# Kernel tuning notes

Hardware: AMD Instinct MI355X
Metric: run time of the kernel (lower is better)

The kernel has to match this reference:

```python
import jax, jax.numpy as jnp
import numpy as np

N = 50000

def gcn_conv(x, src, dst, W, b, num_nodes):
    # x: [N, Fin], src/dst: [E'] (self-loops already included)
    h = x @ W  # [N, Fout]
    ones = jnp.ones(src.shape[0], dtype=h.dtype)
    deg = jax.ops.segment_sum(ones, dst, num_segments=num_nodes)  # in-degree incl. self-loop
    dinv = jnp.where(deg > 0, jax.lax.rsqrt(deg), 0.0)
    norm = dinv[src] * dinv[dst]  # [E']
    msg = h[src] * norm[:, None]  # gather + scale
    out = jax.ops.segment_sum(msg, dst, num_segments=num_nodes)  # scatter-add
    return out + b

def setup_inputs() -> dict:
    key = jax.random.key(0)
    k1, k2, k3, k4, k5, k6 = jax.random.split(key, 6)
    E = 800000
    Fin, H, Fout = 128, 64, 32
    x = jax.random.normal(k1, (N, Fin), dtype=jnp.float32)
    edge_index = jax.random.randint(k2, (2, E), 0, N, dtype=jnp.int32)
    edge_attr = jax.random.normal(k3, (E, 8), dtype=jnp.float32)
    s1 = 1.0 / np.sqrt(Fin)
    s2 = 1.0 / np.sqrt(H)
    W1 = jax.random.uniform(k4, (Fin, H), dtype=jnp.float32, minval=-s1, maxval=s1)
    b1 = jnp.zeros((H,), dtype=jnp.float32)
    W2 = jax.random.uniform(k5, (H, Fout), dtype=jnp.float32, minval=-s2, maxval=s2)
    b2 = jnp.zeros((Fout,), dtype=jnp.float32)
    return {"x": x, "edge_index": edge_index, "edge_attr": edge_attr,
            "W1": W1, "b1": b1, "W2": W2, "b2": b2}

def reference(x, edge_index, edge_attr, W1, b1, W2, b2):
    num_nodes = x.shape[0]
    loop = jnp.arange(num_nodes, dtype=edge_index.dtype)
    src = jnp.concatenate([edge_index[0], loop])
    dst = jnp.concatenate([edge_index[1], loop])
    h = gcn_conv(x, src, dst, W1, b1, num_nodes)
    h = jax.nn.relu(h)
    # dropout is identity in eval mode
    out = gcn_conv(h, src, dst, W2, b2, num_nodes)
    return out
```

## Files before the change

### kernel.cpp

```cpp
#include <hip/hip_runtime.h>
#include <hip/hip_fp16.h>
#include <cstdint>
#include <cstddef>


#define SHIFT 8
#define NPB 256
#define CHUNK 8192
#define IMG_CAP 6144

__global__ __launch_bounds__(256) void hist_kernel(const int* __restrict__ dst, int E, int nWG,
                                                   int B, int* __restrict__ hist) {
  __shared__ int h[256];
  int t = threadIdx.x, w = blockIdx.x;
  for (int i = t; i < B; i += 256) h[i] = 0;
  __syncthreads();
  int beg = w * CHUNK, end = min(beg + CHUNK, E);
  for (int i = beg + t; i < end; i += 256) atomicAdd(&h[dst[i] >> SHIFT], 1);
  __syncthreads();
  for (int i = t; i < B; i += 256) hist[i * nWG + w] = h[i];
}

__global__ __launch_bounds__(256) void rowscan_kernel(const int* __restrict__ hist, int nWG,
                                                      int* __restrict__ rowscan, int* __restrict__ total) {
  int b = blockIdx.x, t = threadIdx.x;
  int v = (t < nWG) ? hist[b * nWG + t] : 0;
  int lane = t & 63, wid = t >> 6;
  int x = v;
#pragma unroll
  for (int o = 1; o < 64; o <<= 1) { int y = __shfl_up(x, o, 64); if (lane >= o) x += y; }
  __shared__ int wsum[4];
  if (lane == 63) wsum[wid] = x;
  __syncthreads();
  int bw = 0;
  for (int i = 0; i < wid; ++i) bw += wsum[i];
  int incl = bw + x;
  if (t < nWG) rowscan[b * nWG + t] = incl - v;
  if (t == nWG - 1) total[b] = incl;
}

__global__ __launch_bounds__(256) void scatterkeys_kernel(const int* __restrict__ src,
                                                          const int* __restrict__ dst, int E, int nWG,
                                                          int B, const int* __restrict__ hist,
                                                          const int* __restrict__ rowscan,
                                                          const int* __restrict__ total,
                                                          unsigned* __restrict__ keys) {
  __shared__ int loffs[256], cur[256], gb[256];
  __shared__ int wsum[4];
  __shared__ unsigned image[CHUNK];
  __shared__ int gdst[CHUNK];
  int t = threadIdx.x, w = blockIdx.x;
  int lane = t & 63, wid = t >> 6;
  {
    int v = (t < B) ? total[t] : 0;
    int x = v;
#pragma unroll
    for (int o = 1; o < 64; o <<= 1) { int y = __shfl_up(x, o, 64); if (lane >= o) x += y; }
    if (lane == 63) wsum[wid] = x;
    __syncthreads();
    int bw = 0;
    for (int i = 0; i < wid; ++i) bw += wsum[i];
    int excl = bw + x - v;
    if (t < B) gb[t] = excl + rowscan[t * nWG + w];
  }
  __syncthreads();
  {
    int v = (t < B) ? hist[t * nWG + w] : 0;
    int x = v;
#pragma unroll
    for (int o = 1; o < 64; o <<= 1) { int y = __shfl_up(x, o, 64); if (lane >= o) x += y; }
    if (lane == 63) wsum[wid] = x;
    __syncthreads();
    int bw = 0;
    for (int i = 0; i < wid; ++i) bw += wsum[i];
    int excl = bw + x - v;
    if (t < B) { loffs[t] = excl; cur[t] = excl; }
  }
  __syncthreads();
  int beg = w * CHUNK, end = min(beg + CHUNK, E);
  for (int i = beg + t; i < end; i += 256) {
    int d = dst[i], s = src[i];
    int b = d >> SHIFT;
    int p = atomicAdd(&cur[b], 1);
    image[p] = ((unsigned)(d & (NPB - 1)) << 16) | (unsigned)s;
    gdst[p] = gb[b] + (p - loffs[b]);
  }
  __syncthreads();
  int n = end - beg;
  for (int i = t; i < n; i += 256) keys[gdst[i]] = image[i];
}

__global__ __launch_bounds__(256) void bucket_build_kernel(const unsigned* __restrict__ keys,
                                                           const int* __restrict__ total, int B, int N,
                                                           int* __restrict__ csr, int* __restrict__ eoff,
                                                           int* __restrict__ ecnt, float* __restrict__ dinv) {
  __shared__ int cnt[NPB], loffs[NPB], cur[NPB];
  __shared__ int red[4];
  __shared__ int image[IMG_CAP];
  int b = blockIdx.x, t = threadIdx.x;
  int lane = t & 63, wid = t >> 6;
  int part = 0;
  for (int i = t; i < b; i += 256) part += total[i];
#pragma unroll
  for (int o = 32; o > 0; o >>= 1) part += __shfl_down(part, o, 64);
  if (lane == 0) red[wid] = part;
  __syncthreads();
  int gbeg = red[0] + red[1] + red[2] + red[3];
  int m = total[b];
  int gend = gbeg + m;
  int nb = b << SHIFT;
  int nn = min(NPB, N - nb);
  cnt[t] = 0;
  __syncthreads();
  for (int i = gbeg + t; i < gend; i += 256) atomicAdd(&cnt[keys[i] >> 16], 1);
  __syncthreads();
  if (t < 64) {
    int v0 = cnt[4 * t], v1 = cnt[4 * t + 1], v2 = cnt[4 * t + 2], v3 = cnt[4 * t + 3];
    int s = v0 + v1 + v2 + v3, x = s;
#pragma unroll
    for (int o = 1; o < 64; o <<= 1) { int y = __shfl_up(x, o, 64); if (t >= o) x += y; }
    int e = x - s;
    loffs[4 * t] = e;                 cur[4 * t] = e;
    loffs[4 * t + 1] = e + v0;        cur[4 * t + 1] = e + v0;
    loffs[4 * t + 2] = e + v0 + v1;   cur[4 * t + 2] = e + v0 + v1;
    loffs[4 * t + 3] = e + v0 + v1 + v2; cur[4 * t + 3] = e + v0 + v1 + v2;
  }
  __syncthreads();
  for (int n2 = t; n2 < nn; n2 += 256) {
    eoff[nb + n2] = gbeg + loffs[n2];
    ecnt[nb + n2] = cnt[n2];
    dinv[nb + n2] = 1.0f / sqrtf((float)(cnt[n2] + 1));
  }
  if (m <= IMG_CAP) {
    for (int i = gbeg + t; i < gend; i += 256) {
      unsigned k = keys[i];
      int p = atomicAdd(&cur[k >> 16], 1);
      image[p] = (int)(k & 0xFFFFu);
    }
    __syncthreads();
    for (int i = t; i < m; i += 256) csr[gbeg + i] = image[i];
  } else {
    for (int i = gbeg + t; i < gend; i += 256) {
      unsigned k = keys[i];
      int p = atomicAdd(&cur[k >> 16], 1);
      csr[gbeg + p] = (int)(k & 0xFFFFu);
    }
  }
}

__global__ __launch_bounds__(256) void gemm1_kernel(
    const float* __restrict__ x, const float* __restrict__ W1,
    const float* __restrict__ dinv, __half* __restrict__ h1s, int N) {
  __shared__ float ws[128 * 64];
  __shared__ float xs[64 * 128];
  const int t = threadIdx.x;
  const int rowBase = blockIdx.x * 64;
  float4* ws4 = (float4*)ws;
  float4* xs4 = (float4*)xs;
  for (int i = t; i < 128 * 16; i += 256) ws4[i] = ((const float4*)W1)[i];
  for (int i = t; i < 64 * 32; i += 256) {
    int r = i >> 5, kq = i & 31;
    int row = rowBase + r;
    float4 v = make_float4(0.f, 0.f, 0.f, 0.f);
    if (row < N) v = ((const float4*)x)[(size_t)row * 32 + kq];
    xs4[r * 32 + (kq ^ ((r >> 2) & 7))] = v;
  }
  __syncthreads();
  const int g = t & 15;
  const int rg = t >> 4;
  const int swz = rg & 7;
  float acc[4][4] = {};
  for (int kq = 0; kq < 32; ++kq) {
    float4 a[4];
#pragma unroll
    for (int j = 0; j < 4; ++j) a[j] = xs4[(4 * rg + j) * 32 + (kq ^ swz)];
    float4 w[4];
#pragma unroll
    for (int kk = 0; kk < 4; ++kk) w[kk] = ws4[(4 * kq + kk) * 16 + g];
#pragma unroll
    for (int j = 0; j < 4; ++j) {
      acc[j][0] += a[j].x * w[0].x + a[j].y * w[1].x + a[j].z * w[2].x + a[j].w * w[3].x;
      acc[j][1] += a[j].x * w[0].y + a[j].y * w[1].y + a[j].z * w[2].y + a[j].w * w[3].y;
      acc[j][2] += a[j].x * w[0].z + a[j].y * w[1].z + a[j].z * w[2].z + a[j].w * w[3].z;
      acc[j][3] += a[j].x * w[0].w + a[j].y * w[1].w + a[j].z * w[2].w + a[j].w * w[3].w;
    }
  }
#pragma unroll
  for (int j = 0; j < 4; ++j) {
    int row = rowBase + 4 * rg + j;
    if (row < N) {
      float dv = dinv[row];
      union { __half2 h2[2]; float2 f2v; } u;
      u.h2[0] = __floats2half2_rn(acc[j][0] * dv, acc[j][1] * dv);
      u.h2[1] = __floats2half2_rn(acc[j][2] * dv, acc[j][3] * dv);
      ((float2*)h1s)[(size_t)row * 16 + g] = u.f2v;
    }
  }
}

__global__ __launch_bounds__(256) void gather64_gemm2_kernel(
    const __half* __restrict__ h1s, const int* __restrict__ csr, const int* __restrict__ eoff,
    const int* __restrict__ ecnt, const float* __restrict__ dinv, const float* __restrict__ b1,
    const float* __restrict__ W2, __half* __restrict__ h2s, int N) {
  __shared__ float w2s[64 * 32];
  __shared__ float arow[8 * 64];
  int t = threadIdx.x;
  float4* w2s4 = (float4*)w2s;
  for (int i = t; i < 512; i += 256) w2s4[i] = ((const float4*)W2)[i];
  __syncthreads();
  int slot = t >> 5;
  int d = blockIdx.x * 8 + slot;
  if (d >= N) return;
  int f2 = t & 31;
  const __half2* h1p = (const __half2*)h1s;
  int beg = eoff[d], m = ecnt[d];
  float2 a0 = __half22float2(h1p[(size_t)d * 32 + f2]);
  float2 aA = make_float2(0.f, 0.f), aB = make_float2(0.f, 0.f), aC = make_float2(0.f, 0.f);
  int j = 0;
  for (; j + 16 <= m; j += 16) {
    int s[16];
#pragma unroll
    for (int i = 0; i < 16; ++i) s[i] = csr[beg + j + i];
    __half2 v[16];
#pragma unroll
    for (int i = 0; i < 16; ++i) v[i] = h1p[(size_t)s[i] * 32 + f2];
#pragma unroll
    for (int i = 0; i < 16; ++i) {
      float2 f = __half22float2(v[i]);
      float2* ac = (i & 3) == 0 ? &a0 : (i & 3) == 1 ? &aA : (i & 3) == 2 ? &aB : &aC;
      ac->x += f.x; ac->y += f.y;
    }
  }
  for (; j + 4 <= m; j += 4) {
    int s0 = csr[beg + j], s1 = csr[beg + j + 1], s2 = csr[beg + j + 2], s3 = csr[beg + j + 3];
    __half2 v0 = h1p[(size_t)s0 * 32 + f2], v1 = h1p[(size_t)s1 * 32 + f2];
    __half2 v2 = h1p[(size_t)s2 * 32 + f2], v3 = h1p[(size_t)s3 * 32 + f2];
    float2 f0 = __half22float2(v0), f1 = __half22float2(v1);
    float2 f2v = __half22float2(v2), f3 = __half22float2(v3);
    a0.x += f0.x; a0.y += f0.y; aA.x += f1.x; aA.y += f1.y;
    aB.x += f2v.x; aB.y += f2v.y; aC.x += f3.x; aC.y += f3.y;
  }
  for (; j < m; ++j) {
    float2 f = __half22float2(h1p[(size_t)csr[beg + j] * 32 + f2]);
    a0.x += f.x; a0.y += f.y;
  }
  float sx = (a0.x + aA.x) + (aB.x + aC.x);
  float sy = (a0.y + aA.y) + (aB.y + aC.y);
  float dv = dinv[d];
  float2 bb = ((const float2*)b1)[f2];
  float ax = fmaxf(sx * dv + bb.x, 0.f);
  float ay = fmaxf(sy * dv + bb.y, 0.f);
  ((float2*)arow)[slot * 32 + f2] = make_float2(ax, ay);
  const float* ar = &arow[slot * 64];
  float s = 0.f;
#pragma unroll
  for (int kk = 0; kk < 64; ++kk) s += ar[kk] * w2s[kk * 32 + f2];
  h2s[(size_t)d * 32 + f2] = __float2half_rn(s * dv);
}

__global__ __launch_bounds__(256) void gather32_kernel(
    const __half* __restrict__ h2s, const int* __restrict__ csr, const int* __restrict__ eoff,
    const int* __restrict__ ecnt, const float* __restrict__ dinv, const float* __restrict__ b2,
    float* __restrict__ out, int N) {
  int t = threadIdx.x;
  int d = blockIdx.x * 16 + (t >> 4);
  if (d >= N) return;
  int f2 = t & 15;
  const __half2* h2p = (const __half2*)h2s;
  int beg = eoff[d], m = ecnt[d];
  float2 a0 = __half22float2(h2p[(size_t)d * 16 + f2]);
  float2 aA = make_float2(0.f, 0.f), aB = make_float2(0.f, 0.f), aC = make_float2(0.f, 0.f);
  int j = 0;
  for (; j + 16 <= m; j += 16) {
    int s[16];
#pragma unroll
    for (int i = 0; i < 16; ++i) s[i] = csr[beg + j + i];
    __half2 v[16];
#pragma unroll
    for (int i = 0; i < 16; ++i) v[i] = h2p[(size_t)s[i] * 16 + f2];
#pragma unroll
    for (int i = 0; i < 16; ++i) {
      float2 f = __half22float2(v[i]);
      float2* ac = (i & 3) == 0 ? &a0 : (i & 3) == 1 ? &aA : (i & 3) == 2 ? &aB : &aC;
      ac->x += f.x; ac->y += f.y;
    }
  }
  for (; j + 4 <= m; j += 4) {
    int s0 = csr[beg + j], s1 = csr[beg + j + 1], s2 = csr[beg + j + 2], s3 = csr[beg + j + 3];
    __half2 v0 = h2p[(size_t)s0 * 16 + f2], v1 = h2p[(size_t)s1 * 16 + f2];
    __half2 v2 = h2p[(size_t)s2 * 16 + f2], v3 = h2p[(size_t)s3 * 16 + f2];
    float2 f0 = __half22float2(v0), f1 = __half22float2(v1);
    float2 f2v = __half22float2(v2), f3 = __half22float2(v3);
    a0.x += f0.x; a0.y += f0.y; aA.x += f1.x; aA.y += f1.y;
    aB.x += f2v.x; aB.y += f2v.y; aC.x += f3.x; aC.y += f3.y;
  }
  for (; j < m; ++j) {
    float2 f = __half22float2(h2p[(size_t)csr[beg + j] * 16 + f2]);
    a0.x += f.x; a0.y += f.y;
  }
  float sx = (a0.x + aA.x) + (aB.x + aC.x);
  float sy = (a0.y + aA.y) + (aB.y + aC.y);
  float dv = dinv[d];
  float2 bb = ((const float2*)b2)[f2];
  ((float2*)out)[(size_t)d * 16 + f2] = make_float2(sx * dv + bb.x, sy * dv + bb.y);
}

extern "C" void kernel_launch(void* const* d_in, const int* in_sizes, int n_in,
                              void* d_out, int out_size, void* d_ws, size_t ws_size,
                              hipStream_t stream) {
  const float* x = (const float*)d_in[0];
  const int* edge_index = (const int*)d_in[1];
  const float* W1 = (const float*)d_in[3];
  const float* b1 = (const float*)d_in[4];
  const float* W2 = (const float*)d_in[5];
  const float* b2 = (const float*)d_in[6];
  float* out = (float*)d_out;

  const int N = in_sizes[0] / 128;
  const int E = in_sizes[1] / 2;
  const int* src = edge_index;
  const int* dst = edge_index + E;

  const int B = (N + NPB - 1) >> SHIFT;
  const int nWG = (E + CHUNK - 1) / CHUNK;

  char* ws = (char*)d_ws;
  size_t off = 0;
  auto alloc = [&](size_t bytes) -> void* {
    void* p = ws + off;
    off += (bytes + 255) & ~(size_t)255;
    return p;
  };
  unsigned* keys = (unsigned*)alloc((size_t)E * 4);
  int* csr = (int*)alloc((size_t)E * 4);
  int* hist = (int*)alloc((size_t)B * nWG * 4);
  int* rowscan = (int*)alloc((size_t)B * nWG * 4);
  int* total = (int*)alloc((size_t)B * 4);
  int* eoff = (int*)alloc((size_t)N * 4);
  int* ecnt = (int*)alloc((size_t)N * 4);
  float* dinv = (float*)alloc((size_t)N * 4);
  __half* h1s = (__half*)alloc((size_t)N * 64 * 2);
  __half* h2s = (__half*)alloc((size_t)N * 32 * 2);

  hist_kernel<<<nWG, 256, 0, stream>>>(dst, E, nWG, B, hist);
  rowscan_kernel<<<B, 256, 0, stream>>>(hist, nWG, rowscan, total);
  scatterkeys_kernel<<<nWG, 256, 0, stream>>>(src, dst, E, nWG, B, hist, rowscan, total, keys);
  bucket_build_kernel<<<B, 256, 0, stream>>>(keys, total, B, N, csr, eoff, ecnt, dinv);
  gemm1_kernel<<<(N + 63) / 64, 256, 0, stream>>>(x, W1, dinv, h1s, N);
  gather64_gemm2_kernel<<<(N + 7) / 8, 256, 0, stream>>>(h1s, csr, eoff, ecnt, dinv, b1, W2, h2s, N);
  gather32_kernel<<<(N + 15) / 16, 256, 0, stream>>>(h2s, csr, eoff, ecnt, dinv, b2, out, N);
}
```

Before: 107.2 us.

## Drop rowscan kernel, use 16-bit CSR indices, widen gather64 loads

Removes the separate rowscan kernel: scatterkeys and bucket_build now recompute bucket totals and prefix offsets by scanning each histogram row themselves. The bucket id is packed into the upper bits of each key, so the gdst shared array is no longer needed, and CHUNK is halved. CSR source indices are stored as 16-bit values, which halves index traffic in both gathers but caps node ids at 65535. gather64 now gives each thread 4 halves per load with 16 threads per node. The cost is redundant serial scans of the histogram row per thread.

```diff
diff --git a/kernel.cpp b/kernel.cpp
--- a/kernel.cpp
+++ b/kernel.cpp
@@ -6,7 +6,7 @@
 
 #define SHIFT 8
 #define NPB 256
-#define CHUNK 8192
+#define CHUNK 4096
 #define IMG_CAP 6144
 
 __global__ __launch_bounds__(256) void hist_kernel(const int* __restrict__ dst, int E, int nWG,
@@ -21,60 +21,45 @@
   for (int i = t; i < B; i += 256) hist[i * nWG + w] = h[i];
 }
 
-__global__ __launch_bounds__(256) void rowscan_kernel(const int* __restrict__ hist, int nWG,
-                                                      int* __restrict__ rowscan, int* __restrict__ total) {
-  int b = blockIdx.x, t = threadIdx.x;
-  int v = (t < nWG) ? hist[b * nWG + t] : 0;
-  int lane = t & 63, wid = t >> 6;
-  int x = v;
-#pragma unroll
-  for (int o = 1; o < 64; o <<= 1) { int y = __shfl_up(x, o, 64); if (lane >= o) x += y; }
-  __shared__ int wsum[4];
-  if (lane == 63) wsum[wid] = x;
-  __syncthreads();
-  int bw = 0;
-  for (int i = 0; i < wid; ++i) bw += wsum[i];
-  int incl = bw + x;
-  if (t < nWG) rowscan[b * nWG + t] = incl - v;
-  if (t == nWG - 1) total[b] = incl;
-}
-
 __global__ __launch_bounds__(256) void scatterkeys_kernel(const int* __restrict__ src,
                                                           const int* __restrict__ dst, int E, int nWG,
                                                           int B, const int* __restrict__ hist,
-                                                          const int* __restrict__ rowscan,
-                                                          const int* __restrict__ total,
                                                           unsigned* __restrict__ keys) {
   __shared__ int loffs[256], cur[256], gb[256];
   __shared__ int wsum[4];
   __shared__ unsigned image[CHUNK];
-  __shared__ int gdst[CHUNK];
   int t = threadIdx.x, w = blockIdx.x;
   int lane = t & 63, wid = t >> 6;
+  int tot = 0, rp = 0, myc = 0;
+  if (t < B) {
+    const int* row = hist + (size_t)t * nWG;
+    for (int w2 = 0; w2 < nWG; ++w2) {
+      int v = row[w2];
+      tot += v;
+      if (w2 < w) rp += v;
+      if (w2 == w) myc = v;
+    }
+  }
   {
-    int v = (t < B) ? total[t] : 0;
-    int x = v;
+    int x = tot;
 #pragma unroll
     for (int o = 1; o < 64; o <<= 1) { int y = __shfl_up(x, o, 64); if (lane >= o) x += y; }
     if (lane == 63) wsum[wid] = x;
     __syncthreads();
     int bw = 0;
     for (int i = 0; i < wid; ++i) bw += wsum[i];
-    int excl = bw + x - v;
-    if (t < B) gb[t] = excl + rowscan[t * nWG + w];
+    if (t < B) gb[t] = bw + x - tot + rp;
   }
   __syncthreads();
   {
-    int v = (t < B) ? hist[t * nWG + w] : 0;
-    int x = v;
+    int x = myc;
 #pragma unroll
     for (int o = 1; o < 64; o <<= 1) { int y = __shfl_up(x, o, 64); if (lane >= o) x += y; }
     if (lane == 63) wsum[wid] = x;
     __syncthreads();
     int bw = 0;
     for (int i = 0; i < wid; ++i) bw += wsum[i];
-    int excl = bw + x - v;
-    if (t < B) { loffs[t] = excl; cur[t] = excl; }
+    if (t < B) { loffs[t] = bw + x - myc; cur[t] = bw + x - myc; }
   }
   __syncthreads();
   int beg = w * CHUNK, end = min(beg + CHUNK, E);
@@ -82,37 +67,51 @@
     int d = dst[i], s = src[i];
     int b = d >> SHIFT;
     int p = atomicAdd(&cur[b], 1);
-    image[p] = ((unsigned)(d & (NPB - 1)) << 16) | (unsigned)s;
-    gdst[p] = gb[b] + (p - loffs[b]);
+    image[p] = ((unsigned)b << 24) | ((unsigned)(d & (NPB - 1)) << 16) | (unsigned)s;
   }
   __syncthreads();
   int n = end - beg;
-  for (int i = t; i < n; i += 256) keys[gdst[i]] = image[i];
+  for (int i = t; i < n; i += 256) {
+    unsigned k = image[i];
+    int b = (int)(k >> 24);
+    keys[gb[b] + (i - loffs[b])] = k;
+  }
 }
 
 __global__ __launch_bounds__(256) void bucket_build_kernel(const unsigned* __restrict__ keys,
-                                                           const int* __restrict__ total, int B, int N,
-                                                           int* __restrict__ csr, int* __restrict__ eoff,
-                                                           int* __restrict__ ecnt, float* __restrict__ dinv) {
+                                                           const int* __restrict__ hist, int nWG,
+                                                           int B, int N,
+                                                           unsigned short* __restrict__ csr,
+                                                           int* __restrict__ eoff,
+                                                           int* __restrict__ ecnt,
+                                                           float* __restrict__ dinv) {
   __shared__ int cnt[NPB], loffs[NPB], cur[NPB];
+  __shared__ int tsum[256];
   __shared__ int red[4];
   __shared__ int image[IMG_CAP];
   int b = blockIdx.x, t = threadIdx.x;
   int lane = t & 63, wid = t >> 6;
+  int tot = 0;
+  if (t < B) {
+    const int* row = hist + (size_t)t * nWG;
+    for (int w2 = 0; w2 < nWG; ++w2) tot += row[w2];
+  }
+  tsum[t] = tot;
+  __syncthreads();
   int part = 0;
-  for (int i = t; i < b; i += 256) part += total[i];
+  for (int i = t; i < b; i += 256) part += tsum[i];
 #pragma unroll
   for (int o = 32; o > 0; o >>= 1) part += __shfl_down(part, o, 64);
   if (lane == 0) red[wid] = part;
   __syncthreads();
   int gbeg = red[0] + red[1] + red[2] + red[3];
-  int m = total[b];
+  int m = tsum[b];
   int gend = gbeg + m;
   int nb = b << SHIFT;
   int nn = min(NPB, N - nb);
   cnt[t] = 0;
   __syncthreads();
-  for (int i = gbeg + t; i < gend; i += 256) atomicAdd(&cnt[keys[i] >> 16], 1);
+  for (int i = gbeg + t; i < gend; i += 256) atomicAdd(&cnt[(keys[i] >> 16) & 0xFF], 1);
   __syncthreads();
   if (t < 64) {
     int v0 = cnt[4 * t], v1 = cnt[4 * t + 1], v2 = cnt[4 * t + 2], v3 = cnt[4 * t + 3];
@@ -134,16 +133,16 @@
   if (m <= IMG_CAP) {
     for (int i = gbeg + t; i < gend; i += 256) {
       unsigned k = keys[i];
-      int p = atomicAdd(&cur[k >> 16], 1);
+      int p = atomicAdd(&cur[(k >> 16) & 0xFF], 1);
       image[p] = (int)(k & 0xFFFFu);
     }
     __syncthreads();
-    for (int i = t; i < m; i += 256) csr[gbeg + i] = image[i];
+    for (int i = t; i < m; i += 256) csr[gbeg + i] = (unsigned short)image[i];
   } else {
     for (int i = gbeg + t; i < gend; i += 256) {
       unsigned k = keys[i];
-      int p = atomicAdd(&cur[k >> 16], 1);
-      csr[gbeg + p] = (int)(k & 0xFFFFu);
+      int p = atomicAdd(&cur[(k >> 16) & 0xFF], 1);
+      csr[gbeg + p] = (unsigned short)(k & 0xFFFFu);
     }
   }
 }
@@ -199,68 +198,91 @@
 }
 
 __global__ __launch_bounds__(256) void gather64_gemm2_kernel(
-    const __half* __restrict__ h1s, const int* __restrict__ csr, const int* __restrict__ eoff,
-    const int* __restrict__ ecnt, const float* __restrict__ dinv, const float* __restrict__ b1,
+    const __half* __restrict__ h1s, const unsigned short* __restrict__ csr,
+    const int* __restrict__ eoff, const int* __restrict__ ecnt,
+    const float* __restrict__ dinv, const float* __restrict__ b1,
     const float* __restrict__ W2, __half* __restrict__ h2s, int N) {
   __shared__ float w2s[64 * 32];
-  __shared__ float arow[8 * 64];
+  __shared__ float arow[16 * 64];
   int t = threadIdx.x;
   float4* w2s4 = (float4*)w2s;
   for (int i = t; i < 512; i += 256) w2s4[i] = ((const float4*)W2)[i];
   __syncthreads();
-  int slot = t >> 5;
-  int d = blockIdx.x * 8 + slot;
+  int slot = t >> 4;
+  int d = blockIdx.x * 16 + slot;
   if (d >= N) return;
-  int f2 = t & 31;
-  const __half2* h1p = (const __half2*)h1s;
+  int f = t & 15;
+  const float2* h1p = (const float2*)h1s;
   int beg = eoff[d], m = ecnt[d];
-  float2 a0 = __half22float2(h1p[(size_t)d * 32 + f2]);
-  float2 aA = make_float2(0.f, 0.f), aB = make_float2(0.f, 0.f), aC = make_float2(0.f, 0.f);
+  float acc[4][4] = {};
+  {
+    union { float2 f2v; __half2 h2[2]; } u;
+    u.f2v = h1p[(size_t)d * 16 + f];
+    float2 lo = __half22float2(u.h2[0]), hi = __half22float2(u.h2[1]);
+    acc[0][0] = lo.x; acc[0][1] = lo.y; acc[0][2] = hi.x; acc[0][3] = hi.y;
+  }
   int j = 0;
   for (; j + 16 <= m; j += 16) {
-    int s[16];
-#pragma unroll
-    for (int i = 0; i < 16; ++i) s[i] = csr[beg + j + i];
-    __half2 v[16];
-#pragma unroll
-    for (int i = 0; i < 16; ++i) v[i] = h1p[(size_t)s[i] * 32 + f2];
+    int s_[16];
+#pragma unroll
+    for (int i = 0; i < 16; ++i) s_[i] = csr[beg + j + i];
+    float2 v_[16];
+#pragma unroll
+    for (int i = 0; i < 16; ++i) v_[i] = h1p[(size_t)s_[i] * 16 + f];
 #pragma unroll
     for (int i = 0; i < 16; ++i) {
-      float2 f = __half22float2(v[i]);
-      float2* ac = (i & 3) == 0 ? &a0 : (i & 3) == 1 ? &aA : (i & 3) == 2 ? &aB : &aC;
-      ac->x += f.x; ac->y += f.y;
+      union { float2 f2v; __half2 h2[2]; } u; u.f2v = v_[i];
+      float2 lo = __half22float2(u.h2[0]), hi = __half22float2(u.h2[1]);
+      acc[i & 3][0] += lo.x; acc[i & 3][1] += lo.y; acc[i & 3][2] += hi.x; acc[i & 3][3] += hi.y;
     }
   }
   for (; j + 4 <= m; j += 4) {
-    int s0 = csr[beg + j], s1 = csr[beg + j + 1], s2 = csr[beg + j + 2], s3 = csr[beg + j + 3];
-    __half2 v0 = h1p[(size_t)s0 * 32 + f2], v1 = h1p[(size_t)s1 * 32 + f2];
-    __half2 v2 = h1p[(size_t)s2 * 32 + f2], v3 = h1p[(size_t)s3 * 32 + f2];
-    float2 f0 = __half22float2(v0), f1 = __half22float2(v1);
-    float2 f2v = __half22float2(v2), f3 = __half22float2(v3);
-    a0.x += f0.x; a0.y += f0.y; aA.x += f1.x; aA.y += f1.y;
-    aB.x += f2v.x; aB.y += f2v.y; aC.x += f3.x; aC.y += f3.y;
+    int s_[4];
+#pragma unroll
+    for (int i = 0; i < 4; ++i) s_[i] = csr[beg + j + i];
+    float2 v_[4];
+#pragma unroll
+    for (int i = 0; i < 4; ++i) v_[i] = h1p[(size_t)s_[i] * 16 + f];
+#pragma unroll
+    for (int i = 0; i < 4; ++i) {
+      union { float2 f2v; __half2 h2[2]; } u; u.f2v = v_[i];
+      float2 lo = __half22float2(u.h2[0]), hi = __half22float2(u.h2[1]);
+      acc[i][0] += lo.x; acc[i][1] += lo.y; acc[i][2] += hi.x; acc[i][3] += hi.y;
+    }
   }
   for (; j < m; ++j) {
-    float2 f = __half22float2(h1p[(size_t)csr[beg + j] * 32 + f2]);
-    a0.x += f.x; a0.y += f.y;
-  }
-  float sx = (a0.x + aA.x) + (aB.x + aC.x);
-  float sy = (a0.y + aA.y) + (aB.y + aC.y);
+    union { float2 f2v; __half2 h2[2]; } u;
+    u.f2v = h1p[(size_t)csr[beg + j] * 16 + f];
+    float2 lo = __half22float2(u.h2[0]), hi = __half22float2(u.h2[1]);
+    acc[0][0] += lo.x; acc[0][1] += lo.y; acc[0][2] += hi.x; acc[0][3] += hi.y;
+  }
+  float g0 = (acc[0][0] + acc[1][0]) + (acc[2][0] + acc[3][0]);
+  float g1 = (acc[0][1] + acc[1][1]) + (acc[2][1] + acc[3][1]);
+  float g2 = (acc[0][2] + acc[1][2]) + (acc[2][2] + acc[3][2]);
+  float g3 = (acc[0][3] + acc[1][3]) + (acc[2][3] + acc[3][3]);
   float dv = dinv[d];
-  float2 bb = ((const float2*)b1)[f2];
-  float ax = fmaxf(sx * dv + bb.x, 0.f);
-  float ay = fmaxf(sy * dv + bb.y, 0.f);
-  ((float2*)arow)[slot * 32 + f2] = make_float2(ax, ay);
+  float4 bb = ((const float4*)b1)[f];
+  float4 a1v;
+  a1v.x = fmaxf(g0 * dv + bb.x, 0.f);
+  a1v.y = fmaxf(g1 * dv + bb.y, 0.f);
+  a1v.z = fmaxf(g2 * dv + bb.z, 0.f);
+  a1v.w = fmaxf(g3 * dv + bb.w, 0.f);
+  ((float4*)arow)[slot * 16 + f] = a1v;
   const float* ar = &arow[slot * 64];
-  float s = 0.f;
-#pragma unroll
-  for (int kk = 0; kk < 64; ++kk) s += ar[kk] * w2s[kk * 32 + f2];
-  h2s[(size_t)d * 32 + f2] = __float2half_rn(s * dv);
+  float s0 = 0.f, s1 = 0.f;
+#pragma unroll
+  for (int kk = 0; kk < 64; ++kk) {
+    float a = ar[kk];
+    float2 wv = ((const float2*)w2s)[kk * 16 + f];
+    s0 += a * wv.x; s1 += a * wv.y;
+  }
+  ((__half2*)h2s)[(size_t)d * 16 + f] = __floats2half2_rn(s0 * dv, s1 * dv);
 }
 
 __global__ __launch_bounds__(256) void gather32_kernel(
-    const __half* __restrict__ h2s, const int* __restrict__ csr, const int* __restrict__ eoff,
-    const int* __restrict__ ecnt, const float* __restrict__ dinv, const float* __restrict__ b2,
+    const __half* __restrict__ h2s, const unsigned short* __restrict__ csr,
+    const int* __restrict__ eoff, const int* __restrict__ ecnt,
+    const float* __restrict__ dinv, const float* __restrict__ b2,
     float* __restrict__ out, int N) {
   int t = threadIdx.x;
   int d = blockIdx.x * 16 + (t >> 4);
@@ -272,15 +294,15 @@
   float2 aA = make_float2(0.f, 0.f), aB = make_float2(0.f, 0.f), aC = make_float2(0.f, 0.f);
   int j = 0;
   for (; j + 16 <= m; j += 16) {
-    int s[16];
-#pragma unroll
-    for (int i = 0; i < 16; ++i) s[i] = csr[beg + j + i];
-    __half2 v[16];
-#pragma unroll
-    for (int i = 0; i < 16; ++i) v[i] = h2p[(size_t)s[i] * 16 + f2];
+    int s_[16];
+#pragma unroll
+    for (int i = 0; i < 16; ++i) s_[i] = csr[beg + j + i];
+    __half2 v_[16];
+#pragma unroll
+    for (int i = 0; i < 16; ++i) v_[i] = h2p[(size_t)s_[i] * 16 + f2];
 #pragma unroll
     for (int i = 0; i < 16; ++i) {
-      float2 f = __half22float2(v[i]);
+      float2 f = __half22float2(v_[i]);
       float2* ac = (i & 3) == 0 ? &a0 : (i & 3) == 1 ? &aA : (i & 3) == 2 ? &aB : &aC;
       ac->x += f.x; ac->y += f.y;
     }
@@ -332,10 +354,8 @@
     return p;
   };
   unsigned* keys = (unsigned*)alloc((size_t)E * 4);
-  int* csr = (int*)alloc((size_t)E * 4);
+  unsigned short* csr = (unsigned short*)alloc((size_t)E * 2);
   int* hist = (int*)alloc((size_t)B * nWG * 4);
-  int* rowscan = (int*)alloc((size_t)B * nWG * 4);
-  int* total = (int*)alloc((size_t)B * 4);
   int* eoff = (int*)alloc((size_t)N * 4);
   int* ecnt = (int*)alloc((size_t)N * 4);
   float* dinv = (float*)alloc((size_t)N * 4);
@@ -343,10 +363,9 @@
   __half* h2s = (__half*)alloc((size_t)N * 32 * 2);
 
   hist_kernel<<<nWG, 256, 0, stream>>>(dst, E, nWG, B, hist);
-  rowscan_kernel<<<B, 256, 0, stream>>>(hist, nWG, rowscan, total);
-  scatterkeys_kernel<<<nWG, 256, 0, stream>>>(src, dst, E, nWG, B, hist, rowscan, total, keys);
-  bucket_build_kernel<<<B, 256, 0, stream>>>(keys, total, B, N, csr, eoff, ecnt, dinv);
+  scatterkeys_kernel<<<nWG, 256, 0, stream>>>(src, dst, E, nWG, B, hist, keys);
+  bucket_build_kernel<<<B, 256, 0, stream>>>(keys, hist, nWG, B, N, csr, eoff, ecnt, dinv);
   gemm1_kernel<<<(N + 63) / 64, 256, 0, stream>>>(x, W1, dinv, h1s, N);
-  gather64_gemm2_kernel<<<(N + 7) / 8, 256, 0, stream>>>(h1s, csr, eoff, ecnt, dinv, b1, W2, h2s, N);
+  gather64_gemm2_kernel<<<(N + 15) / 16, 256, 0, stream>>>(h1s, csr, eoff, ecnt, dinv, b1, W2, h2s, N);
   gather32_kernel<<<(N + 15) / 16, 256, 0, stream>>>(h2s, csr, eoff, ecnt, dinv, b2, out, N);
 }
```

After: 128.8 us. +20.1%, slower.
